# Kernel tuning notes

Measured on AMD Instinct MI355X. Metric: run time of the kernel, lower is better.

The kernel has to match this reference:

```python
import jax, jax.numpy as jnp
import numpy as np

B, L, D = 4, 2048, 512


def setup_inputs() -> dict:
    key = jax.random.key(0)
    ks = jax.random.split(key, 12)
    f32 = jnp.float32
    mk = lambda k, s: jax.random.normal(k, s, dtype=f32)
    # xavier-uniform-ish init scale for the linear weights
    w_qkv_lim = np.sqrt(6.0 / (6 * D + 6 * D)).astype(np.float32)
    w_out_lim = np.sqrt(6.0 / (2 * D + 2 * D)).astype(np.float32)
    return {
        "q_real": mk(ks[0], (B, L, D)),
        "q_imag": mk(ks[1], (B, L, D)),
        "k_real": mk(ks[2], (B, L, D)),
        "k_imag": mk(ks[3], (B, L, D)),
        "v_real": mk(ks[4], (B, L, D)),
        "v_imag": mk(ks[5], (B, L, D)),
        "pad_mask": jax.random.randint(ks[6], (B, L), 0, 2).astype(jnp.bool_),
        "W_qkv": jax.random.uniform(ks[7], (6 * D, 6 * D), f32, -w_qkv_lim, w_qkv_lim),
        "b_qkv": jnp.zeros((6 * D,), f32),
        "W_out": jax.random.uniform(ks[8], (2 * D, 2 * D), f32, -w_out_lim, w_out_lim),
        "b_out": jnp.zeros((2 * D,), f32),
    }


def reference(q_real, q_imag, k_real, k_imag, v_real, v_imag, pad_mask,
              W_qkv, b_qkv, W_out, b_out):
    b, l, d = q_real.shape
    # fused QKV projection over concatenated real/imag streams: [B, L, 6D]
    x = jnp.concatenate([q_real, q_imag, k_real, k_imag, v_real, v_imag], axis=-1)
    qkv = x @ W_qkv.T + b_qkv                      # torch Linear: x @ W^T + b
    qkv = qkv.reshape(b, l, 6, d)
    q_r, k_r = qkv[:, :, 0], qkv[:, :, 2]
    v_r, v_i = qkv[:, :, 4], qkv[:, :, 5]
    scale = jnp.asarray(d, jnp.float32) ** -0.5
    scores = jnp.einsum('bqd,bkd->bqk', q_r, k_r) * scale   # [B, L, L]
    scores = jnp.where(pad_mask[:, None, :], -jnp.inf, scores)
    attn = jax.nn.softmax(scores, axis=-1)         # dropout omitted (eval mode)
    out_real = jnp.einsum('bqk,bkd->bqd', attn, v_r)
    out_imag = jnp.einsum('bqk,bkd->bqd', attn, v_i)
    out = jnp.concatenate([out_real, out_imag], axis=-1) @ W_out.T + b_out
    return out[..., :d], out[..., d:]
```

## Files before the change

### kernel.cpp

```cpp
#include <hip/hip_runtime.h>
#include <cstdint>
#include <cstddef>

typedef unsigned short ushort;
typedef __attribute__((ext_vector_type(8))) short short8;
typedef __attribute__((ext_vector_type(16))) float f32x16;

__device__ __forceinline__ float bf2f(ushort u) {
  union { unsigned u; float f; } c; c.u = ((unsigned)u) << 16; return c.f;
}
__device__ __forceinline__ ushort f2bf(float f) {
  union { float f; unsigned u; } c; c.f = f;
  unsigned u = c.u;
  return (ushort)((u + 0x7fffu + ((u >> 16) & 1u)) >> 16);
}

#define G2L(g, l) __builtin_amdgcn_global_load_lds( \
    (const __attribute__((address_space(1))) void*)(g), \
    (__attribute__((address_space(3))) void*)(l), 16, 0, 0)

struct MArgs {
  const ushort* A; int lda; long asz;
  const ushort* B; int ldb; long bsz;
  void* C; int ldc; long csz;
  int K;
  const float* bias;
  float* C2;
};

template<int MODE>
__launch_bounds__(256)
__global__ void mfma_gemm(MArgs g) {
  __shared__ ushort As[128 * 64];
  __shared__ ushort Bs[128 * 64];
  const int tid = threadIdx.x;
  const int lane = tid & 63;
  const int wave = tid >> 6;
  const int z = blockIdx.z;
  const long m0 = (long)blockIdx.y * 128;
  const long n0 = (long)blockIdx.x * 128;
  const ushort* A = g.A + (long)z * g.asz;
  const ushort* B = g.B + (long)z * g.bsz;

  const int srow = tid >> 3;
  const int sk = ((((tid & 7) - (srow & 7)) & 7)) * 8;
  const ushort* ga[4]; const ushort* gb[4];
  ushort* la[4]; ushort* lb[4];
#pragma unroll
  for (int gp = 0; gp < 4; ++gp) {
    ga[gp] = A + (m0 + gp * 32 + srow) * g.lda + sk;
    gb[gp] = B + (n0 + gp * 32 + srow) * g.ldb + sk;
    la[gp] = As + gp * 2048 + tid * 8;
    lb[gp] = Bs + gp * 2048 + tid * 8;
  }

  const int wm = (wave >> 1) * 64;
  const int wn = (wave & 1) * 64;
  const int fr = lane & 31;
  const ushort* rA = As + (wm + fr) * 64;
  const ushort* rB = Bs + (wn + fr) * 64;
  const int cbase = ((lane >> 5) + (lane & 7)) & 7;
  int offk[4];
#pragma unroll
  for (int h = 0; h < 4; ++h) offk[h] = ((cbase + 2 * h) & 7) * 8;

  f32x16 acc[2][2];
#pragma unroll
  for (int i = 0; i < 2; ++i)
#pragma unroll
    for (int j = 0; j < 2; ++j)
#pragma unroll
      for (int r = 0; r < 16; ++r) acc[i][j][r] = 0.f;

  for (int k0 = 0; k0 < g.K; k0 += 64) {
#pragma unroll
    for (int gp = 0; gp < 4; ++gp) G2L(ga[gp] + k0, la[gp]);
#pragma unroll
    for (int gp = 0; gp < 4; ++gp) G2L(gb[gp] + k0, lb[gp]);
    __syncthreads();
#pragma unroll
    for (int h = 0; h < 4; ++h) {
      short8 a0 = *(const short8*)(rA + offk[h]);
      short8 a1 = *(const short8*)(rA + 2048 + offk[h]);
      short8 b0 = *(const short8*)(rB + offk[h]);
      short8 b1 = *(const short8*)(rB + 2048 + offk[h]);
      acc[0][0] = __builtin_amdgcn_mfma_f32_32x32x16_bf16(a0, b0, acc[0][0], 0, 0, 0);
      acc[0][1] = __builtin_amdgcn_mfma_f32_32x32x16_bf16(a0, b1, acc[0][1], 0, 0, 0);
      acc[1][0] = __builtin_amdgcn_mfma_f32_32x32x16_bf16(a1, b0, acc[1][0], 0, 0, 0);
      acc[1][1] = __builtin_amdgcn_mfma_f32_32x32x16_bf16(a1, b1, acc[1][1], 0, 0, 0);
    }
    __syncthreads();
  }

  const int cc = lane & 31;
  const int rbase = 4 * (lane >> 5);
  ushort* Cu = (ushort*)g.C + (long)z * g.csz;
  float* Cf = (float*)g.C;
#pragma unroll
  for (int mt = 0; mt < 2; ++mt) {
#pragma unroll
    for (int nt = 0; nt < 2; ++nt) {
      const long col = n0 + wn + nt * 32 + cc;
      float bv = 0.f;
      if (MODE == 0 || MODE == 3) bv = g.bias[col];
#pragma unroll
      for (int r = 0; r < 16; ++r) {
        const long row = m0 + wm + mt * 32 + (r & 3) + 8 * (r >> 2) + rbase;
        float v = acc[mt][nt][r] + bv;
        if (MODE == 3) {
          float* dst = (col < 512) ? (Cf + row * 512 + col) : (g.C2 + row * 512 + (col - 512));
          *dst = v;
        } else {
          Cu[row * (long)g.ldc + col] = f2bf(v);
        }
      }
    }
  }
}

__global__ void cvt_x6(const float* x0, const float* x1, const float* x2,
                       const float* x3, const float* x4, const float* x5, ushort* X) {
  const long m = blockIdx.y;
  const int c4 = (blockIdx.x * 256 + threadIdx.x) * 4;
  const int p = c4 >> 9, d = c4 & 511;
  const float* xp;
  switch (p) {
    case 0: xp = x0; break; case 1: xp = x1; break; case 2: xp = x2; break;
    case 3: xp = x3; break; case 4: xp = x4; break; default: xp = x5; break;
  }
  float4 v = *(const float4*)(xp + m * 512 + d);
  ushort4 o; o.x = f2bf(v.x); o.y = f2bf(v.y); o.z = f2bf(v.z); o.w = f2bf(v.w);
  *(ushort4*)(X + m * 3072 + c4) = o;
}

__device__ __forceinline__ int chunk_map(int c) { return (c == 0) ? 0 : (c == 1) ? 2 : (c == 2) ? 4 : 5; }

__global__ void cvt_w4(const float* W, ushort* Wq4) {
  const long r = blockIdx.y;
  const int c4 = (blockIdx.x * 256 + threadIdx.x) * 4;
  const long wr = (long)chunk_map((int)(r >> 9)) * 512 + (r & 511);
  float4 v = *(const float4*)(W + wr * 3072 + c4);
  ushort4 o; o.x = f2bf(v.x); o.y = f2bf(v.y); o.z = f2bf(v.z); o.w = f2bf(v.w);
  *(ushort4*)(Wq4 + r * 3072 + c4) = o;
}

__global__ void cvt_wout(const float* W, ushort* Wo) {
  const long r = blockIdx.y;
  const int c4 = threadIdx.x * 4;
  float4 v = *(const float4*)(W + r * 1024 + c4);
  ushort4 o; o.x = f2bf(v.x); o.y = f2bf(v.y); o.z = f2bf(v.z); o.w = f2bf(v.w);
  *(ushort4*)(Wo + r * 1024 + c4) = o;
}

__global__ void mk_bias4(const float* bqkv, float* b4) {
  const int n = blockIdx.x * 256 + threadIdx.x;
  b4[n] = bqkv[chunk_map(n >> 9) * 512 + (n & 511)];
}

__global__ void transpose_v(const ushort* QKV, ushort* Vt) {
  __shared__ ushort t[64][65];
  const int tid = threadIdx.x;
  const int k0 = blockIdx.x * 64, n0 = blockIdx.y * 64, b = blockIdx.z;
  const ushort* src = QKV + (long)b * 2048 * 2048 + 1024;
#pragma unroll
  for (int i = 0; i < 16; ++i) {
    int idx = i * 256 + tid; int r = idx >> 6, c = idx & 63;
    t[r][c] = src[(long)(k0 + r) * 2048 + (n0 + c)];
  }
  __syncthreads();
  ushort* dst = Vt + (long)b * 1024 * 2048;
#pragma unroll
  for (int i = 0; i < 16; ++i) {
    int idx = i * 256 + tid; int r = idx >> 6, c = idx & 63;
    dst[(long)(n0 + r) * 2048 + (k0 + c)] = t[c][r];
  }
}

__launch_bounds__(256)
__global__ void softmax_rows(ushort* S, const int* mask) {
  const int lane = threadIdx.x & 63;
  const int wave = threadIdx.x >> 6;
  const long row = (long)blockIdx.x * 4 + wave;
  const int* m = mask + (row >> 11) * 2048 + lane * 32;
  ushort* s = S + row * 2048 + lane * 32;
  const float scale = 0.04419417382415922f;

  short8 raw[4];
#pragma unroll
  for (int i = 0; i < 4; ++i) raw[i] = *(const short8*)(s + i * 8);
  int4 mi[8];
#pragma unroll
  for (int i = 0; i < 8; ++i) mi[i] = *(const int4*)(m + i * 4);

  float v[32];
  int mk[32];
#pragma unroll
  for (int i = 0; i < 8; ++i) {
    mk[i * 4 + 0] = mi[i].x; mk[i * 4 + 1] = mi[i].y;
    mk[i * 4 + 2] = mi[i].z; mk[i * 4 + 3] = mi[i].w;
  }
#pragma unroll
  for (int i = 0; i < 32; ++i) v[i] = bf2f((ushort)raw[i >> 3][i & 7]) * scale;

  float mx = -INFINITY;
#pragma unroll
  for (int i = 0; i < 32; ++i) if (!mk[i]) mx = fmaxf(mx, v[i]);
#pragma unroll
  for (int off = 32; off; off >>= 1) mx = fmaxf(mx, __shfl_xor(mx, off));

  float sum = 0.f;
#pragma unroll
  for (int i = 0; i < 32; ++i) {
    float e = mk[i] ? 0.f : __expf(v[i] - mx);
    v[i] = e;
    sum += e;
  }
#pragma unroll
  for (int off = 32; off; off >>= 1) sum += __shfl_xor(sum, off);

  float r = 1.f / sum;
  short8 out[4];
#pragma unroll
  for (int i = 0; i < 32; ++i) out[i >> 3][i & 7] = (short)f2bf(v[i] * r);
#pragma unroll
  for (int i = 0; i < 4; ++i) *(short8*)(s + i * 8) = out[i];
}

extern "C" void kernel_launch(void* const* d_in, const int* in_sizes, int n_in,
                              void* d_out, int out_size, void* d_ws, size_t ws_size,
                              hipStream_t stream) {
  const float* qr = (const float*)d_in[0];
  const float* qi = (const float*)d_in[1];
  const float* kr = (const float*)d_in[2];
  const float* ki = (const float*)d_in[3];
  const float* vr = (const float*)d_in[4];
  const float* vi = (const float*)d_in[5];
  const int* pm = (const int*)d_in[6];
  const float* Wqkv = (const float*)d_in[7];
  const float* bqkv = (const float*)d_in[8];
  const float* Wout = (const float*)d_in[9];
  const float* bout = (const float*)d_in[10];
  float* out = (float*)d_out;

  char* base = (char*)d_ws;
  ushort* QKV   = (ushort*)(base);
  ushort* Wq4   = (ushort*)(base + 33554432);
  ushort* Wo    = (ushort*)(base + 46137344);
  float*  b4    = (float*) (base + 48234496);
  char*   uni   = base + 48242688;
  ushort* Xbf   = (ushort*)(uni);
  ushort* Vt    = (ushort*)(uni);
  ushort* S     = (ushort*)(uni + 16777216);
  ushort* AO    = (ushort*)(uni + 50331648);

  cvt_x6<<<dim3(3, 8192), 256, 0, stream>>>(qr, qi, kr, ki, vr, vi, Xbf);
  cvt_w4<<<dim3(3, 2048), 256, 0, stream>>>(Wqkv, Wq4);
  cvt_wout<<<dim3(1, 1024), 256, 0, stream>>>(Wout, Wo);
  mk_bias4<<<8, 256, 0, stream>>>(bqkv, b4);

  {
    MArgs a{};
    a.A = Xbf; a.lda = 3072; a.asz = 0;
    a.B = Wq4; a.ldb = 3072; a.bsz = 0;
    a.C = QKV; a.ldc = 2048; a.csz = 0;
    a.K = 3072; a.bias = b4;
    mfma_gemm<0><<<dim3(16, 64, 1), 256, 0, stream>>>(a);
  }

  transpose_v<<<dim3(32, 16, 4), 256, 0, stream>>>(QKV, Vt);

  {
    MArgs a{};
    a.A = QKV;        a.lda = 2048; a.asz = (long)2048 * 2048;
    a.B = QKV + 512;  a.ldb = 2048; a.bsz = (long)2048 * 2048;
    a.C = S;          a.ldc = 2048; a.csz = (long)2048 * 2048;
    a.K = 512;
    mfma_gemm<1><<<dim3(16, 16, 4), 256, 0, stream>>>(a);
  }

  softmax_rows<<<2048, 256, 0, stream>>>(S, pm);

  {
    MArgs a{};
    a.A = S;  a.lda = 2048; a.asz = (long)2048 * 2048;
    a.B = Vt; a.ldb = 2048; a.bsz = (long)1024 * 2048;
    a.C = AO; a.ldc = 1024; a.csz = (long)2048 * 1024;
    a.K = 2048;
    mfma_gemm<2><<<dim3(8, 16, 4), 256, 0, stream>>>(a);
  }

  {
    MArgs a{};
    a.A = AO; a.lda = 1024; a.asz = 0;
    a.B = Wo; a.ldb = 1024; a.bsz = 0;
    a.C = out; a.ldc = 512; a.csz = 0;
    a.C2 = out + (long)8192 * 512;
    a.K = 1024; a.bias = bout;
    mfma_gemm<3><<<dim3(8, 64, 1), 256, 0, stream>>>(a);
  }
}
```

Before: 430.2 us.

## Double-buffer GEMM LDS loads with larger 256-row tiles and grid swizzle

Rewrites the MFMA GEMM as a 512-thread kernel with 256xBN tiles, double-buffered LDS stages prefetched two iterations ahead using vmcnt-based waits instead of full syncthreads, raised wave priority during MFMA, and a workgroup index remap for L2 locality. It aims to hide global-to-LDS latency and raise arithmetic intensity per block. In exchange it doubles LDS use (up to 128KB at BN=256), which limits occupancy, and the small attention GEMMs get fewer blocks, which may underfill the CUs.

```diff
diff --git a/kernel.cpp b/kernel.cpp
--- a/kernel.cpp
+++ b/kernel.cpp
@@ -28,85 +28,133 @@
   float* C2;
 };
 
-template<int MODE>
-__launch_bounds__(256)
+template<int MODE, int BN>
+__launch_bounds__(512, 2)
 __global__ void mfma_gemm(MArgs g) {
-  __shared__ ushort As[128 * 64];
-  __shared__ ushort Bs[128 * 64];
+  constexpr int BM = 256;
+  constexpr int WN = BN / 64;
+  constexpr int WM = 8 / WN;
+  constexpr int WMSZ = BM / WM;
+  constexpr int MF = WMSZ / 32;
+  constexpr int NBG = BN / 64;
+  constexpr int LPS = 4 + NBG;
+
+  __shared__ __attribute__((aligned(16))) ushort As[2][BM * 64];
+  __shared__ __attribute__((aligned(16))) ushort Bs[2][BN * 64];
+
   const int tid = threadIdx.x;
   const int lane = tid & 63;
   const int wave = tid >> 6;
   const int z = blockIdx.z;
-  const long m0 = (long)blockIdx.y * 128;
-  const long n0 = (long)blockIdx.x * 128;
-  const ushort* A = g.A + (long)z * g.asz;
-  const ushort* B = g.B + (long)z * g.bsz;
+
+  int bx = blockIdx.x, by = blockIdx.y;
+  {
+    const int gx = gridDim.x;
+    const int nwg = gx * gridDim.y;
+    int wg = by * gx + bx;
+    wg = (wg & 7) * (nwg >> 3) + (wg >> 3);
+    bx = wg % gx; by = wg / gx;
+  }
+  const long m0 = (long)by * BM;
+  const long n0 = (long)bx * BN;
+  const ushort* Ab = g.A + (long)z * g.asz;
+  const ushort* Bb = g.B + (long)z * g.bsz;
 
   const int srow = tid >> 3;
-  const int sk = ((((tid & 7) - (srow & 7)) & 7)) * 8;
-  const ushort* ga[4]; const ushort* gb[4];
-  ushort* la[4]; ushort* lb[4];
-#pragma unroll
-  for (int gp = 0; gp < 4; ++gp) {
-    ga[gp] = A + (m0 + gp * 32 + srow) * g.lda + sk;
-    gb[gp] = B + (n0 + gp * 32 + srow) * g.ldb + sk;
-    la[gp] = As + gp * 2048 + tid * 8;
-    lb[gp] = Bs + gp * 2048 + tid * 8;
-  }
-
-  const int wm = (wave >> 1) * 64;
-  const int wn = (wave & 1) * 64;
-  const int fr = lane & 31;
-  const ushort* rA = As + (wm + fr) * 64;
-  const ushort* rB = Bs + (wn + fr) * 64;
-  const int cbase = ((lane >> 5) + (lane & 7)) & 7;
-  int offk[4];
-#pragma unroll
-  for (int h = 0; h < 4; ++h) offk[h] = ((cbase + 2 * h) & 7) * 8;
-
-  f32x16 acc[2][2];
-#pragma unroll
-  for (int i = 0; i < 2; ++i)
-#pragma unroll
-    for (int j = 0; j < 2; ++j)
-#pragma unroll
-      for (int r = 0; r < 16; ++r) acc[i][j][r] = 0.f;
-
-  for (int k0 = 0; k0 < g.K; k0 += 64) {
-#pragma unroll
-    for (int gp = 0; gp < 4; ++gp) G2L(ga[gp] + k0, la[gp]);
-#pragma unroll
-    for (int gp = 0; gp < 4; ++gp) G2L(gb[gp] + k0, lb[gp]);
-    __syncthreads();
+  const long skel = (long)((((tid & 7) - srow) & 7) * 8);
+  const ushort* ga[4];
+  const ushort* gb[NBG];
+#pragma unroll
+  for (int q = 0; q < 4; ++q) ga[q] = Ab + (m0 + q * 64 + srow) * (long)g.lda + skel;
+#pragma unroll
+  for (int q = 0; q < NBG; ++q) gb[q] = Bb + (n0 + q * 64 + srow) * (long)g.ldb + skel;
+
+  const int l31 = lane & 31, hb = lane >> 5;
+  const int wmi = wave / WN, wni = wave % WN;
+  int aoff[MF], arot[MF];
+#pragma unroll
+  for (int mf = 0; mf < MF; ++mf) {
+    const int r = wmi * WMSZ + mf * 32 + l31;
+    aoff[mf] = r * 64;
+    arot[mf] = (r + hb) & 7;
+  }
+  int boff[2], brot[2];
+#pragma unroll
+  for (int nf = 0; nf < 2; ++nf) {
+    const int r = wni * 64 + nf * 32 + l31;
+    boff[nf] = r * 64;
+    brot[nf] = (r + hb) & 7;
+  }
+
+  f32x16 acc[MF][2];
+#pragma unroll
+  for (int mf = 0; mf < MF; ++mf)
+#pragma unroll
+    for (int nf = 0; nf < 2; ++nf)
+#pragma unroll
+      for (int r = 0; r < 16; ++r) acc[mf][nf][r] = 0.f;
+
+  auto STAGEF = [&](int buf, int t) {
+    const long ko = (long)t * 64;
+#pragma unroll
+    for (int q = 0; q < 4; ++q) G2L(ga[q] + ko, &As[buf][q * 4096 + tid * 8]);
+#pragma unroll
+    for (int q = 0; q < NBG; ++q) G2L(gb[q] + ko, &Bs[buf][q * 4096 + tid * 8]);
+  };
+
+  STAGEF(0, 0);
+  STAGEF(1, 1);
+
+  const int nt = g.K >> 6;
+  int cur = 0;
+  for (int t = 0; t < nt; ++t) {
+    if (t + 1 < nt) asm volatile("s_waitcnt vmcnt(%0)" :: "n"(LPS) : "memory");
+    else            asm volatile("s_waitcnt vmcnt(0)" ::: "memory");
+    __builtin_amdgcn_s_barrier();
+    asm volatile("" ::: "memory");
+
+    const ushort* as = &As[cur][0];
+    const ushort* bs = &Bs[cur][0];
+    __builtin_amdgcn_s_setprio(1);
 #pragma unroll
     for (int h = 0; h < 4; ++h) {
-      short8 a0 = *(const short8*)(rA + offk[h]);
-      short8 a1 = *(const short8*)(rA + 2048 + offk[h]);
-      short8 b0 = *(const short8*)(rB + offk[h]);
-      short8 b1 = *(const short8*)(rB + 2048 + offk[h]);
-      acc[0][0] = __builtin_amdgcn_mfma_f32_32x32x16_bf16(a0, b0, acc[0][0], 0, 0, 0);
-      acc[0][1] = __builtin_amdgcn_mfma_f32_32x32x16_bf16(a0, b1, acc[0][1], 0, 0, 0);
-      acc[1][0] = __builtin_amdgcn_mfma_f32_32x32x16_bf16(a1, b0, acc[1][0], 0, 0, 0);
-      acc[1][1] = __builtin_amdgcn_mfma_f32_32x32x16_bf16(a1, b1, acc[1][1], 0, 0, 0);
+      short8 av[MF], bv[2];
+#pragma unroll
+      for (int mf = 0; mf < MF; ++mf)
+        av[mf] = *(const short8*)(as + aoff[mf] + (((2 * h + arot[mf]) & 7) << 3));
+#pragma unroll
+      for (int nf = 0; nf < 2; ++nf)
+        bv[nf] = *(const short8*)(bs + boff[nf] + (((2 * h + brot[nf]) & 7) << 3));
+#pragma unroll
+      for (int mf = 0; mf < MF; ++mf)
+#pragma unroll
+        for (int nf = 0; nf < 2; ++nf)
+          acc[mf][nf] = __builtin_amdgcn_mfma_f32_32x32x16_bf16(av[mf], bv[nf], acc[mf][nf], 0, 0, 0);
     }
-    __syncthreads();
-  }
-
-  const int cc = lane & 31;
-  const int rbase = 4 * (lane >> 5);
+    __builtin_amdgcn_s_setprio(0);
+
+    asm volatile("s_waitcnt lgkmcnt(0)" ::: "memory");
+    __builtin_amdgcn_s_barrier();
+    asm volatile("" ::: "memory");
+    if (t + 2 < nt) STAGEF(cur, t + 2);
+    cur ^= 1;
+  }
+
+  const int cc = l31;
+  const int rbase = 4 * hb;
   ushort* Cu = (ushort*)g.C + (long)z * g.csz;
   float* Cf = (float*)g.C;
 #pragma unroll
-  for (int mt = 0; mt < 2; ++mt) {
-#pragma unroll
-    for (int nt = 0; nt < 2; ++nt) {
-      const long col = n0 + wn + nt * 32 + cc;
-      float bv = 0.f;
-      if (MODE == 0 || MODE == 3) bv = g.bias[col];
+  for (int mf = 0; mf < MF; ++mf) {
+#pragma unroll
+    for (int nf = 0; nf < 2; ++nf) {
+      const long col = n0 + wni * 64 + nf * 32 + cc;
+      float bsv = 0.f;
+      if (MODE == 0 || MODE == 3) bsv = g.bias[col];
 #pragma unroll
       for (int r = 0; r < 16; ++r) {
-        const long row = m0 + wm + mt * 32 + (r & 3) + 8 * (r >> 2) + rbase;
-        float v = acc[mt][nt][r] + bv;
+        const long row = m0 + wmi * WMSZ + mf * 32 + (r & 3) + 8 * (r >> 2) + rbase;
+        float v = acc[mf][nf][r] + bsv;
         if (MODE == 3) {
           float* dst = (col < 512) ? (Cf + row * 512 + col) : (g.C2 + row * 512 + (col - 512));
           *dst = v;
@@ -264,7 +312,7 @@
     a.B = Wq4; a.ldb = 3072; a.bsz = 0;
     a.C = QKV; a.ldc = 2048; a.csz = 0;
     a.K = 3072; a.bias = b4;
-    mfma_gemm<0><<<dim3(16, 64, 1), 256, 0, stream>>>(a);
+    mfma_gemm<0, 256><<<dim3(8, 32, 1), 512, 0, stream>>>(a);
   }
 
   transpose_v<<<dim3(32, 16, 4), 256, 0, stream>>>(QKV, Vt);
@@ -275,7 +323,7 @@
     a.B = QKV + 512;  a.ldb = 2048; a.bsz = (long)2048 * 2048;
     a.C = S;          a.ldc = 2048; a.csz = (long)2048 * 2048;
     a.K = 512;
-    mfma_gemm<1><<<dim3(16, 16, 4), 256, 0, stream>>>(a);
+    mfma_gemm<1, 256><<<dim3(8, 8, 4), 512, 0, stream>>>(a);
   }
 
   softmax_rows<<<2048, 256, 0, stream>>>(S, pm);
@@ -286,7 +334,7 @@
     a.B = Vt; a.ldb = 2048; a.bsz = (long)1024 * 2048;
     a.C = AO; a.ldc = 1024; a.csz = (long)2048 * 1024;
     a.K = 2048;
-    mfma_gemm<2><<<dim3(8, 16, 4), 256, 0, stream>>>(a);
+    mfma_gemm<2, 128><<<dim3(8, 8, 4), 512, 0, stream>>>(a);
   }
 
   {
@@ -296,6 +344,6 @@
     a.C = out; a.ldc = 512; a.csz = 0;
     a.C2 = out + (long)8192 * 512;
     a.K = 1024; a.bias = bout;
-    mfma_gemm<3><<<dim3(8, 64, 1), 256, 0, stream>>>(a);
-  }
-}
+    mfma_gemm<3, 128><<<dim3(8, 32, 1), 512, 0, stream>>>(a);
+  }
+}
```

Measured after the change: 409.4 us. 4.8% less time.
